# Optimization experiments

Measured on AMD Instinct MI355X. Metric: run time of the kernel, lower is better.

The kernel has to match this reference:

```python
import jax, jax.numpy as jnp
import numpy as np
import math

NHEADS = 4


def _mab(Q, K, qw, qb, kw, kb, vw, vb, ow, ob, mask):
    """MAB2 from tripletformer: multi-head attention (head split via cat(split,0)),
    softmax scale uses sqrt(FULL dim_V), masked_fill(mask==0, -1e10), residual on
    the projected Q, then O + relu(fc_o(O))."""
    dv = qw.shape[1]
    dh = dv // NHEADS
    B, Nq, _ = Q.shape
    Nk = K.shape[1]
    Qh = (Q @ qw + qb).reshape(B, Nq, NHEADS, dh).transpose(0, 2, 1, 3)  # B,h,Nq,dh
    Kh = (K @ kw + kb).reshape(B, Nk, NHEADS, dh).transpose(0, 2, 1, 3)
    Vh = (K @ vw + vb).reshape(B, Nk, NHEADS, dh).transpose(0, 2, 1, 3)
    att = jnp.einsum('bhqd,bhkd->bhqk', Qh, Kh) * (1.0 / math.sqrt(dv))
    att = jnp.where(mask, att, jnp.asarray(-1e10, att.dtype))
    A = jax.nn.softmax(att, axis=-1)
    Oh = Qh + jnp.einsum('bhqk,bhkd->bhqd', A, Vh)
    O = Oh.transpose(0, 2, 1, 3).reshape(B, Nq, dv)
    return O + jax.nn.relu(O @ ow + ob)


def _forward(context_x, value, mask, obs_len, iff_w, iff_b, ind_points,
             q0w, q0b, k0w, k0b, v0w, v0b, o0w, o0b,
             q1w, q1b, k1w, k1b, v1w, v1b, o1w, o1b):
    B, L = context_x.shape
    D = value.shape[-1]
    mflat = mask.reshape(B, L * D)
    # stable stream compaction: observed entries first, original (time-major,
    # channel-minor) order preserved; truncate to static obs_len
    order = jnp.argsort(-mflat, axis=-1, stable=True)[:, :obs_len]  # (B, N)
    T = jnp.broadcast_to(context_x[:, :, None], (B, L, D)).reshape(B, L * D)
    C = jnp.broadcast_to(jnp.arange(D, dtype=jnp.int32), (B, L, D)).reshape(B, L * D)
    U = value.reshape(B, L * D)
    take = lambda a: jnp.take_along_axis(a, order, axis=-1)
    T_, U_, mk_ = take(T), take(U), take(mflat)
    Ch = jax.nn.one_hot(take(C), D, dtype=value.dtype)  # one_hot(num_classes=dim-2)
    X = jnp.concatenate([Ch, T_[..., None], U_[..., None]], axis=-1) * mk_[..., None]
    Y = jax.nn.relu(X @ iff_w + iff_b) * mk_[..., None]
    key_valid = mk_ > 0                        # (B, N)
    mask1 = key_valid[:, None, None, :]        # mab0: mask padded keys
    mask2 = key_valid[:, None, :, None]        # mab1: mask padded query rows
    Z = Y
    n_layers = ind_points.shape[0]
    for i in range(n_layers):
        I = jnp.broadcast_to(ind_points[i], (B,) + ind_points[i].shape)
        H = _mab(I, Z, q0w[i], q0b[i], k0w[i], k0b[i], v0w[i], v0b[i], o0w[i], o0b[i], mask1)
        Zn = _mab(Z, H, q1w[i], q1b[i], k1w[i], k1b[i], v1w[i], v1b[i], o1w[i], o1b[i], mask2)
        Z = Zn * mk_[..., None] + Z
    return Z, mk_[..., None]


def setup_inputs() -> dict:
    B, L, D, OBS, DK, M, NL = 16, 512, 41, 4096, 128, 128, 3
    key = jax.random.key(0)
    ks = jax.random.split(key, 16)
    context_x = jnp.sort(jax.random.uniform(ks[0], (B, L), dtype=jnp.float32), axis=-1)
    value = jax.random.normal(ks[1], (B, L, D), dtype=jnp.float32)
    # exactly OBS observed entries per batch row -> static packed length
    r = jax.random.uniform(ks[2], (B, L * D))
    kth = jnp.sort(r, axis=-1)[:, OBS]
    mask = (r < kth[:, None]).astype(jnp.float32).reshape(B, L, D)

    def w(k, shape, fan):
        return jax.random.normal(k, shape, dtype=jnp.float32) / math.sqrt(fan)

    inp = dict(
        context_x=context_x, value=value, mask=mask, obs_len=OBS,
        iff_w=w(ks[3], (D + 2, DK), D + 2), iff_b=jnp.zeros((DK,), jnp.float32),
        ind_points=w(ks[4], (NL, M, DK), DK),
    )
    for j, n in enumerate(['q0', 'k0', 'v0', 'o0', 'q1', 'k1', 'v1', 'o1']):
        inp[n + 'w'] = w(ks[5 + j], (NL, DK, DK), DK)
        inp[n + 'b'] = jnp.zeros((NL, DK), jnp.float32)
    return inp


def reference(context_x, value, mask, obs_len, iff_w, iff_b, ind_points,
              q0w, q0b, k0w, k0b, v0w, v0b, o0w, o0b,
              q1w, q1b, k1w, k1b, v1w, v1b, o1w, o1b):
    return _forward(context_x, value, mask, obs_len, iff_w, iff_b, ind_points,
                    q0w, q0b, k0w, k0b, v0w, v0b, o0w, o0b,
                    q1w, q1b, k1w, k1b, v1w, v1b, o1w, o1b)
```

## Files before the change

### kernel.cpp

```cpp
#include <hip/hip_runtime.h>
#include <math.h>

#define NBATCH 16
#define SEQL   512
#define DIM    41
#define LDFLAT (SEQL*DIM)
#define OBS    4096
#define DK     128
#define NH     4
#define DH     32

typedef short bf16x8 __attribute__((ext_vector_type(8)));
typedef short short8v __attribute__((ext_vector_type(8)));
typedef float floatx4 __attribute__((ext_vector_type(4)));

__device__ __forceinline__ short f2bf(float f) {
  union { float f; unsigned u; } v;
  v.f = f;
  unsigned r = (v.u + 0x7fffu + ((v.u >> 16) & 1u)) >> 16;
  return (short)r;
}
__device__ __forceinline__ float bf2f(short s) {
  union { unsigned u; float f; } v;
  v.u = ((unsigned)(unsigned short)s) << 16;
  return v.f;
}


__device__ __forceinline__ int swz(int row, int col) {
  return row * 128 + ((((col >> 3) ^ row) & 15) << 3) + (col & 7);
}

typedef struct { int4 v[4]; } WStageH;
__device__ __forceinline__ void stage_load_h(WStageH& s,
                                             const short* __restrict__ Wh,
                                             int tid) {
#pragma unroll
  for (int k = 0; k < 4; k++)
    s.v[k] = *(const int4*)&Wh[(size_t)tid * 8 + (size_t)k * 2048];
}
__device__ __forceinline__ void stage_write_h(short* Wl, const WStageH& s,
                                              int tid) {
#pragma unroll
  for (int k = 0; k < 4; k++) {
    int i = tid * 8 + k * 2048;
    *(int4*)&Wl[swz(i >> 7, i & 127)] = s.v[k];
  }
}
typedef struct { int4 v[2]; } WStageF;
__device__ __forceinline__ void stage_load_f(WStageF& s,
                                             const short* __restrict__ W,
                                             int tid) {
#pragma unroll
  for (int k = 0; k < 2; k++)
    s.v[k] = *(const int4*)&W[(size_t)tid * 8 + (size_t)k * 8192];
}
__device__ __forceinline__ void stage_write_f(short* Wl, const WStageF& s,
                                              int tid) {
#pragma unroll
  for (int k = 0; k < 2; k++) {
    int i = tid * 8 + k * 8192;
    *(int4*)&Wl[swz(i >> 7, i & 127)] = s.v[k];
  }
}

__device__ __forceinline__ void gemm4_s(const short* Wl, const bf16x8 af[4],
                                        int lm, int quad, floatx4 acc[4]) {
#pragma unroll
  for (int nt = 0; nt < 4; nt++) acc[nt] = (floatx4){0.f, 0.f, 0.f, 0.f};
#pragma unroll
  for (int kc = 0; kc < 4; kc++) {
    bf16x8 a = af[kc];
#pragma unroll
    for (int nt = 0; nt < 4; nt++) {
      bf16x8 b = *(const bf16x8*)&Wl[swz(nt * 16 + lm, kc * 32 + quad * 8)];
      acc[nt] = __builtin_amdgcn_mfma_f32_16x16x32_bf16(a, b, acc[nt], 0, 0, 0);
    }
  }
}
__device__ __forceinline__ void gemm2_s(const short* Wl, const bf16x8 af[4],
                                        int colq, int lm, int quad,
                                        floatx4 acc[2]) {
#pragma unroll
  for (int nt = 0; nt < 2; nt++) acc[nt] = (floatx4){0.f, 0.f, 0.f, 0.f};
#pragma unroll
  for (int kc = 0; kc < 4; kc++) {
    bf16x8 a = af[kc];
#pragma unroll
    for (int nt = 0; nt < 2; nt++) {
      bf16x8 b = *(const bf16x8*)&Wl[swz(colq * 32 + nt * 16 + lm,
                                         kc * 32 + quad * 8)];
      acc[nt] = __builtin_amdgcn_mfma_f32_16x16x32_bf16(a, b, acc[nt], 0, 0, 0);
    }
  }
}
__device__ __forceinline__ void load_af_s(const short* Xl, int strip, int lm,
                                          int quad, bf16x8 af[4]) {
#pragma unroll
  for (int kc = 0; kc < 4; kc++)
    af[kc] = *(const bf16x8*)&Xl[swz(strip * 16 + lm, kc * 32 + quad * 8)];
}
__device__ __forceinline__ void store_sl4(short* Sl, const floatx4 acc[4],
                                          const float* __restrict__ bias,
                                          int wv, int lm, int quad,
                                          int colbase) {
#pragma unroll
  for (int nt = 0; nt < 4; nt++) {
    int col = colbase + nt * 16 + lm;
    float bn = bias[col];
#pragma unroll
    for (int r = 0; r < 4; r++)
      Sl[swz(wv * 16 + quad * 4 + r, col)] = f2bf(acc[nt][r] + bn);
  }
}
__device__ __forceinline__ void write_hs_s(const short* Sl,
                                           short* __restrict__ out, int rb,
                                           int nshift, int tid) {
  int rr = tid >> 2, hh = tid & 3;
  int r = rb + rr;
  int bb = r >> nshift, nn = r & ((1 << nshift) - 1);
  size_t o = (((size_t)(bb * NH + hh) << nshift) + nn) * 32;
#pragma unroll
  for (int j = 0; j < 4; j++)
    *(int4*)&out[o + j * 8] = *(int4*)&Sl[swz(rr, hh * 32 + j * 8)];
}
__device__ __forceinline__ void write_hs_q(const short* Sl,
                                           short* __restrict__ out, int rb,
                                           int nshift, int strip, int colq,
                                           int lane) {
  int rr = strip * 16 + (lane >> 2);
  int r = rb + rr;
  int bb = r >> nshift, nn = r & ((1 << nshift) - 1);
  size_t o = (((size_t)(bb * NH + colq) << nshift) + nn) * 32 + (lane & 3) * 8;
  *(int4*)&out[o] = *(const int4*)&Sl[swz(rr, colq * 32 + (lane & 3) * 8)];
}

__global__ __launch_bounds__(1024) void prep_build_kernel(
    const float* __restrict__ q0w, const float* __restrict__ k0w,
    const float* __restrict__ v0w, const float* __restrict__ o0w,
    const float* __restrict__ q1w, const float* __restrict__ k1w,
    const float* __restrict__ v1w, const float* __restrict__ o1w,
    short* __restrict__ Wt,
    const float* __restrict__ mask, int* __restrict__ order,
    float* __restrict__ mk_out, float* __restrict__ mk_out2) {
  __shared__ float Tl[128 * 132];
  __shared__ int c_ones[21];
  __shared__ int base_ones[21];
  __shared__ int base_zeros[21];
  __shared__ int s_total;
  int tid = threadIdx.x;

  if (blockIdx.x < 24) {
    int id = blockIdx.x, l = id >> 3, wi = id & 7;
    const float* s;
    switch (wi) {
      case 0: s = q0w; break; case 1: s = k0w; break;
      case 2: s = v0w; break; case 3: s = o0w; break;
      case 4: s = q1w; break; case 5: s = k1w; break;
      case 6: s = v1w; break; default: s = o1w; break;
    }
    s += (size_t)l * 16384;
    for (int i = tid * 4; i < 16384; i += 4096) {
      int k = i >> 7, n = i & 127;
      float4 x = *(const float4*)&s[i];
      Tl[k * 132 + n + 0] = x.x; Tl[k * 132 + n + 1] = x.y;
      Tl[k * 132 + n + 2] = x.z; Tl[k * 132 + n + 3] = x.w;
    }
    __syncthreads();
    short* dst = Wt + (size_t)id * 16384;
    int n = tid >> 3, k0 = (tid & 7) * 16;
    for (int jc = 0; jc < 2; jc++) {
      short8v t;
#pragma unroll
      for (int j = 0; j < 8; j++) t[j] = f2bf(Tl[(k0 + jc * 8 + j) * 132 + n]);
      *(short8v*)&dst[n * 128 + k0 + jc * 8] = t;
    }
    return;
  }

  int b = blockIdx.x - 24;
  const float* m = mask + (size_t)b * LDFLAT;
  int lane = tid & 63, w = tid >> 6;

  for (int ch = w; ch < 21; ch += 16) {
    int cnt = 0;
    for (int off = lane; off < 1024; off += 64) {
      int j = ch * 1024 + off;
      if (j < LDFLAT) cnt += (m[j] > 0.f) ? 1 : 0;
    }
    for (int o = 32; o > 0; o >>= 1) cnt += __shfl_xor(cnt, o);
    if (lane == 0) c_ones[ch] = cnt;
  }
  __syncthreads();
  if (tid == 0) {
    int ro = 0, rz = 0, tot = 0;
    for (int ch = 0; ch < 21; ch++) tot += c_ones[ch];
    for (int ch = 0; ch < 21; ch++) {
      base_ones[ch] = ro; base_zeros[ch] = rz;
      int cv = (ch == 20) ? (LDFLAT - 20 * 1024) : 1024;
      ro += c_ones[ch]; rz += cv - c_ones[ch];
    }
    s_total = tot;
  }
  __syncthreads();
  int total_ones = s_total;
  for (int ch = w; ch < 21; ch += 16) {
    int obase = base_ones[ch], zbase = base_zeros[ch];
    int climit = (ch == 20) ? (LDFLAT - 20 * 1024) : 1024;
    int run_ones = 0;
    for (int off0 = 0; off0 < climit; off0 += 64) {
      int off = off0 + lane;
      bool valid = off < climit;
      int j = ch * 1024 + off;
      float mv = valid ? m[j] : 0.f;
      int one = (valid && mv > 0.f) ? 1 : 0;
      int v = one;
      for (int o = 1; o < 64; o <<= 1) {
        int t = __shfl_up(v, (unsigned)o);
        if (lane >= o) v += t;
      }
      int wave_ones = __shfl(v, 63);
      if (valid) {
        int ones_before = run_ones + (v - one);
        int pos = one ? (obase + ones_before)
                      : (total_ones + zbase + (off - ones_before));
        if (pos < OBS) {
          order[b * OBS + pos] = j;
          mk_out[b * OBS + pos] = mv;
          mk_out2[b * OBS + pos] = mv;
        }
      }
      run_ones += wave_ones;
    }
  }
}

__global__ __launch_bounds__(256, 3) void fusedA_kernel(
    const int* __restrict__ order, const float* __restrict__ mk_g,
    const float* __restrict__ cx, const float* __restrict__ value,
    const float* __restrict__ iff_w, const float* __restrict__ iff_b,
    float* __restrict__ Z,
    const short* __restrict__ Wk, const float* __restrict__ kbias,
    short* __restrict__ Kb,
    const short* __restrict__ Wv, const float* __restrict__ vbias,
    short* __restrict__ Vb,
    const short* __restrict__ Wq, const float* __restrict__ qbias,
    short* __restrict__ Qb,
    const float* __restrict__ indp, const short* __restrict__ WtAll,
    const float* __restrict__ q0b_all, short* __restrict__ qh_b) {
  __shared__ __align__(16) short Xl[64 * 128];
  __shared__ __align__(16) short WlA[64 * 128];
  __shared__ __align__(16) short WlB[64 * 128];
  int tid = threadIdx.x;
  int wv = tid >> 6, lane = tid & 63, lm = lane & 15, quad = lane >> 4;
  int r_l = lane >> 2, seg = lane & 3;
  int lrow = wv * 16 + r_l;

  if (blockIdx.x >= 1024) {
    int id = blockIdx.x - 1024;
    int l = id >> 1, rbq = (id & 1) * 64;
    const float* X = indp + (size_t)l * 16384 + (size_t)rbq * 128;
    const short* W = WtAll + (size_t)(l * 8) * 16384;
    const float* bias = q0b_all + (size_t)l * 128;
    short* out = qh_b + (size_t)l * 16384;
    WStageH sA, sB;
    stage_load_h(sA, W, tid);
    stage_load_h(sB, W + 8192, tid);
    const float* Xr = X + (size_t)lrow * 128;
#pragma unroll
    for (int jj = 0; jj < 8; jj++) {
      int col = seg * 32 + jj * 4;
      float4 x = *(const float4*)&Xr[col];
      *(short4*)&Xl[swz(lrow, col)] =
          make_short4(f2bf(x.x), f2bf(x.y), f2bf(x.z), f2bf(x.w));
    }
    stage_write_h(WlA, sA, tid);
    stage_write_h(WlB, sB, tid);
    __syncthreads();
    bf16x8 af[4];
    load_af_s(Xl, wv, lm, quad, af);
    floatx4 acc[4];
    gemm4_s(WlA, af, lm, quad, acc);
    store_sl4(Xl, acc, bias, wv, lm, quad, 0);
    gemm4_s(WlB, af, lm, quad, acc);
    store_sl4(Xl, acc, bias, wv, lm, quad, 64);
    write_hs_s(Xl, out, rbq, 7, tid);
    return;
  }

  int rb = blockIdx.x * 64;
  WStageH s0; stage_load_h(s0, Wk, tid);
  int grow = rb + lrow;
  int bb = grow >> 12;
  int j = order[grow];
  int l = j / DIM, d = j - l * DIM;
  float t = cx[bb * SEQL + l];
  float u = value[(size_t)bb * LDFLAT + j];
  float mkv = mk_g[grow];
#pragma unroll
  for (int jj = 0; jj < 8; jj++) {
    int col = seg * 32 + jj * 4;
    float4 w0 = *(const float4*)&iff_w[d * DK + col];
    float4 w1 = *(const float4*)&iff_w[41 * DK + col];
    float4 w2 = *(const float4*)&iff_w[42 * DK + col];
    float4 b4 = *(const float4*)&iff_b[col];
    float4 z;
    z.x = fmaxf(w0.x + t * w1.x + u * w2.x + b4.x, 0.f) * mkv;
    z.y = fmaxf(w0.y + t * w1.y + u * w2.y + b4.y, 0.f) * mkv;
    z.z = fmaxf(w0.z + t * w1.z + u * w2.z + b4.z, 0.f) * mkv;
    z.w = fmaxf(w0.w + t * w1.w + u * w2.w + b4.w, 0.f) * mkv;
    *(float4*)&Z[(size_t)grow * DK + col] = z;
    *(short4*)&Xl[swz(lrow, col)] =
        make_short4(f2bf(z.x), f2bf(z.y), f2bf(z.z), f2bf(z.w));
  }
  stage_write_h(WlA, s0, tid);
  __syncthreads();
  WStageH s1; stage_load_h(s1, Wk + 8192, tid);
  bf16x8 af[4];
  load_af_s(Xl, wv, lm, quad, af);
  floatx4 acc[4];
  gemm4_s(WlA, af, lm, quad, acc);
  store_sl4(Xl, acc, kbias, wv, lm, quad, 0);
  stage_write_h(WlB, s1, tid);
  __syncthreads();
  WStageH s2; stage_load_h(s2, Wv, tid);
  gemm4_s(WlB, af, lm, quad, acc);
  store_sl4(Xl, acc, kbias, wv, lm, quad, 64);
  write_hs_s(Xl, Kb, rb, 12, tid);
  stage_write_h(WlA, s2, tid);
  __syncthreads();
  WStageH s3; stage_load_h(s3, Wv + 8192, tid);
  gemm4_s(WlA, af, lm, quad, acc);
  store_sl4(Xl, acc, vbias, wv, lm, quad, 0);
  stage_write_h(WlB, s3, tid);
  __syncthreads();
  WStageH s4; stage_load_h(s4, Wq, tid);
  gemm4_s(WlB, af, lm, quad, acc);
  store_sl4(Xl, acc, vbias, wv, lm, quad, 64);
  write_hs_s(Xl, Vb, rb, 12, tid);
  stage_write_h(WlA, s4, tid);
  __syncthreads();
  WStageH s5; stage_load_h(s5, Wq + 8192, tid);
  gemm4_s(WlA, af, lm, quad, acc);
  store_sl4(Xl, acc, qbias, wv, lm, quad, 0);
  stage_write_h(WlB, s5, tid);
  __syncthreads();
  gemm4_s(WlB, af, lm, quad, acc);
  store_sl4(Xl, acc, qbias, wv, lm, quad, 64);
  write_hs_s(Xl, Qb, rb, 12, tid);
}

__global__ __launch_bounds__(256) void attn1_kernel(
    const short* __restrict__ Qh,
    const short* __restrict__ Kh, const short* __restrict__ Vh,
    const float* __restrict__ mk,
    float* __restrict__ Opart, float* __restrict__ mpart,
    float* __restrict__ lpart) {
  __shared__ __align__(16) short Ql[128 * 40];
  __shared__ __align__(16) short Kc[64 * 40];
  __shared__ __align__(16) short Vtc[32 * 74];
  __shared__ __align__(16) short Pl[128 * 72];
  __shared__ float mkc[64];
  int bh = blockIdx.x;
  int b = bh >> 2, h = bh & 3;
  int ks = blockIdx.y;
  int tid = threadIdx.x;
  int wv = tid >> 6, lane = tid & 63, lm = lane & 15, quad = lane >> 4;

  const float scale = 0.08838834764831845f;
  const short* kbase = Kh + ((size_t)bh * OBS + ks * 512) * 32;
  const short* vbase = Vh + ((size_t)bh * OBS + ks * 512) * 32;
  const float* mkb = mk + (size_t)b * OBS + ks * 512;

  int i0 = tid * 8;
  int r0 = i0 >> 5, cv = i0 & 31;
  int4 kreg = *(const int4*)&kbase[i0];
  int4 vreg = *(const int4*)&vbase[i0];
  float mreg = (tid < 64) ? mkb[tid] : 0.f;

  const short* qbg = Qh + (size_t)h * 128 * 32;
  for (int i = tid * 8; i < 128 * 32; i += 2048) {
    int r = i >> 5, c = i & 31;
    *(int4*)&Ql[r * 40 + c] = *(const int4*)&qbg[i];
  }
  __syncthreads();
  bf16x8 aq[2];
  aq[0] = *(bf16x8*)&Ql[(wv * 32 + lm) * 40 + quad * 8];
  aq[1] = *(bf16x8*)&Ql[(wv * 32 + 16 + lm) * 40 + quad * 8];

  float m_i[2][4], l_i[2][4];
  floatx4 oacc[2][2];
#pragma unroll
  for (int mt = 0; mt < 2; mt++) {
#pragma unroll
    for (int r = 0; r < 4; r++) { m_i[mt][r] = -1e30f; l_i[mt][r] = 0.f; }
    oacc[mt][0] = (floatx4){0.f, 0.f, 0.f, 0.f};
    oacc[mt][1] = (floatx4){0.f, 0.f, 0.f, 0.f};
  }

  for (int ch = 0; ch < 8; ch++) {
    __syncthreads();
    *(int4*)&Kc[r0 * 40 + cv] = kreg;
    {
      short* vv = (short*)&vreg;
#pragma unroll
      for (int j = 0; j < 8; j++) Vtc[(cv + j) * 74 + r0] = vv[j];
    }
    if (tid < 64) mkc[tid] = mreg;
    if (ch < 7) {
      kreg = *(const int4*)&kbase[(ch + 1) * 2048 + i0];
      vreg = *(const int4*)&vbase[(ch + 1) * 2048 + i0];
      if (tid < 64) mreg = mkb[(ch + 1) * 64 + tid];
    }
    __syncthreads();

    floatx4 sf[2][4];
#pragma unroll
    for (int nt = 0; nt < 4; nt++) {
      bf16x8 bfrag = *(bf16x8*)&Kc[(nt * 16 + lm) * 40 + quad * 8];
      floatx4 z = {0.f, 0.f, 0.f, 0.f};
      sf[0][nt] = __builtin_amdgcn_mfma_f32_16x16x32_bf16(aq[0], bfrag, z, 0, 0, 0);
      sf[1][nt] = __builtin_amdgcn_mfma_f32_16x16x32_bf16(aq[1], bfrag, z, 0, 0, 0);
    }
#pragma unroll
    for (int nt = 0; nt < 4; nt++) {
      float mkv = mkc[nt * 16 + lm];
      bool ok = mkv > 0.f;
#pragma unroll
      for (int mt = 0; mt < 2; mt++)
#pragma unroll
        for (int r = 0; r < 4; r++)
          sf[mt][nt][r] = ok ? sf[mt][nt][r] * scale : -1e10f;
    }
#pragma unroll
    for (int mt = 0; mt < 2; mt++) {
#pragma unroll
      for (int r = 0; r < 4; r++) {
        float mx = fmaxf(fmaxf(sf[mt][0][r], sf[mt][1][r]),
                         fmaxf(sf[mt][2][r], sf[mt][3][r]));
        mx = fmaxf(mx, __shfl_xor(mx, 1));
        mx = fmaxf(mx, __shfl_xor(mx, 2));
        mx = fmaxf(mx, __shfl_xor(mx, 4));
        mx = fmaxf(mx, __shfl_xor(mx, 8));
        float mn = fmaxf(m_i[mt][r], mx);
        float al = __expf(m_i[mt][r] - mn);
        float ps = 0.f;
#pragma unroll
        for (int nt = 0; nt < 4; nt++) {
          float p = __expf(sf[mt][nt][r] - mn);
          sf[mt][nt][r] = p;
          ps += p;
        }
        ps += __shfl_xor(ps, 1);
        ps += __shfl_xor(ps, 2);
        ps += __shfl_xor(ps, 4);
        ps += __shfl_xor(ps, 8);
        l_i[mt][r] = l_i[mt][r] * al + ps;
        m_i[mt][r] = mn;
        oacc[mt][0] *= al;
        oacc[mt][1] *= al;
      }
    }
#pragma unroll
    for (int mt = 0; mt < 2; mt++)
#pragma unroll
      for (int nt = 0; nt < 4; nt++)
#pragma unroll
        for (int r = 0; r < 4; r++)
          Pl[(wv * 32 + mt * 16 + quad * 4 + r) * 72 + nt * 16 + lm] =
              f2bf(sf[mt][nt][r]);
#pragma unroll
    for (int kc = 0; kc < 2; kc++) {
      bf16x8 vf0 = *(bf16x8*)&Vtc[lm * 74 + kc * 32 + quad * 8];
      bf16x8 vf1 = *(bf16x8*)&Vtc[(16 + lm) * 74 + kc * 32 + quad * 8];
#pragma unroll
      for (int mt = 0; mt < 2; mt++) {
        bf16x8 pf = *(bf16x8*)&Pl[(wv * 32 + mt * 16 + lm) * 72 + kc * 32 + quad * 8];
        oacc[mt][0] = __builtin_amdgcn_mfma_f32_16x16x32_bf16(pf, vf0, oacc[mt][0], 0, 0, 0);
        oacc[mt][1] = __builtin_amdgcn_mfma_f32_16x16x32_bf16(pf, vf1, oacc[mt][1], 0, 0, 0);
      }
    }
  }
  float* ob = Opart + (size_t)(ks * 64 + bh) * 128 * 32;
#pragma unroll
  for (int mt = 0; mt < 2; mt++) {
#pragma unroll
    for (int r = 0; r < 4; r++) {
      int row = wv * 32 + mt * 16 + quad * 4 + r;
      ob[(size_t)row * 32 + lm] = oacc[mt][0][r];
      ob[(size_t)row * 32 + 16 + lm] = oacc[mt][1][r];
      if (lm == 0) {
        mpart[(size_t)(ks * 64 + bh) * 128 + row] = m_i[mt][r];
        lpart[(size_t)(ks * 64 + bh) * 128 + row] = l_i[mt][r];
      }
    }
  }
}

__global__ __launch_bounds__(1024) void fusedB_kernel(
    const float* __restrict__ Opart, const float* __restrict__ mpart,
    const float* __restrict__ lpart, const short* __restrict__ qh,
    const short* __restrict__ Wo, const float* __restrict__ obias,
    const short* __restrict__ Wk, const float* __restrict__ kbias,
    const short* __restrict__ Wv, const float* __restrict__ vbias,
    short* __restrict__ khb, short* __restrict__ vhb) {
  __shared__ __align__(16) short Xl[64 * 128];
  __shared__ __align__(16) short WlA[128 * 128];
  __shared__ __align__(16) short WlB[128 * 128];
  int tid = threadIdx.x;
  int rb = blockIdx.x * 64;
  int b = rb >> 7, n0 = rb & 127;
  int wv = tid >> 6, lane = tid & 63, lm = lane & 15, quad = lane >> 4;
  int strip = wv & 3, colq = wv >> 2;
  WStageF sWo; stage_load_f(sWo, Wo, tid);
#pragma unroll
  for (int p = 0; p < 2; p++) {
    int slot = p * 1024 + tid;
    int pair = slot >> 3;
    int hh = pair & 3, rr = pair >> 2;
    int c4 = (slot & 7) * 4;
    int n = n0 + rr;
    int bh = b * 4 + hh;
    float mv[8], lv[8], m = -1e30f;
#pragma unroll
    for (int s = 0; s < 8; s++) {
      mv[s] = mpart[(size_t)(s * 64 + bh) * 128 + n];
      lv[s] = lpart[(size_t)(s * 64 + bh) * 128 + n];
      m = fmaxf(m, mv[s]);
    }
    float l = 0.f, oa0 = 0.f, oa1 = 0.f, oa2 = 0.f, oa3 = 0.f;
#pragma unroll
    for (int s = 0; s < 8; s++) {
      float w = __expf(mv[s] - m);
      l += lv[s] * w;
      float4 v = *(const float4*)&Opart[((size_t)(s * 64 + bh) * 128 + n) * 32 + c4];
      oa0 += v.x * w; oa1 += v.y * w; oa2 += v.z * w; oa3 += v.w * w;
    }
    float li = 1.f / l;
    int2 qi = *(const int2*)&qh[((size_t)hh * 128 + n) * 32 + c4];
    const short* qs = (const short*)&qi;
    short4 o4;
    o4.x = f2bf(bf2f(qs[0]) + oa0 * li);
    o4.y = f2bf(bf2f(qs[1]) + oa1 * li);
    o4.z = f2bf(bf2f(qs[2]) + oa2 * li);
    o4.w = f2bf(bf2f(qs[3]) + oa3 * li);
    *(short4*)&Xl[swz(rr, hh * 32 + c4)] = o4;
  }
  stage_write_f(WlA, sWo, tid);
  __syncthreads();
  bf16x8 afO[4];
  load_af_s(Xl, strip, lm, quad, afO);
  __syncthreads();
  WStageF sWk; stage_load_f(sWk, Wk, tid);
  floatx4 acc[2];
  gemm2_s(WlA, afO, colq, lm, quad, acc);
#pragma unroll
  for (int nt = 0; nt < 2; nt++) {
    int col = colq * 32 + nt * 16 + lm;
    float bn = obias[col];
#pragma unroll
    for (int r = 0; r < 4; r++) {
      int row = strip * 16 + quad * 4 + r;
      float ov = bf2f(Xl[swz(row, col)]);
      Xl[swz(row, col)] = f2bf(ov + fmaxf(acc[nt][r] + bn, 0.f));
    }
  }
  stage_write_f(WlB, sWk, tid);
  __syncthreads();
  bf16x8 afH[4];
  load_af_s(Xl, strip, lm, quad, afH);
  __syncthreads();
  WStageF sWv; stage_load_f(sWv, Wv, tid);
  gemm2_s(WlB, afH, colq, lm, quad, acc);
#pragma unroll
  for (int nt = 0; nt < 2; nt++) {
    int col = colq * 32 + nt * 16 + lm;
    float bn = kbias[col];
#pragma unroll
    for (int r = 0; r < 4; r++)
      Xl[swz(strip * 16 + quad * 4 + r, col)] = f2bf(acc[nt][r] + bn);
  }
  write_hs_q(Xl, khb, rb, 7, strip, colq, lane);
  stage_write_f(WlA, sWv, tid);
  __syncthreads();
  gemm2_s(WlA, afH, colq, lm, quad, acc);
#pragma unroll
  for (int nt = 0; nt < 2; nt++) {
    int col = colq * 32 + nt * 16 + lm;
    float bn = vbias[col];
#pragma unroll
    for (int r = 0; r < 4; r++)
      Xl[swz(strip * 16 + quad * 4 + r, col)] = f2bf(acc[nt][r] + bn);
  }
  write_hs_q(Xl, vhb, rb, 7, strip, colq, lane);
}

__global__ __launch_bounds__(256, 4) void attn2_kernel(
    const short* __restrict__ Qh, const short* __restrict__ Kh,
    const short* __restrict__ Vh, short* __restrict__ O) {
  __shared__ __align__(16) short Kl[128 * 40];
  __shared__ __align__(16) short Vt[32 * 136];
  __shared__ __align__(16) short Ql[64 * 40];
  __shared__ __align__(16) short Pl[64 * 128];
  int bh = blockIdx.x;
  int b = bh >> 2, h = bh & 3;
  int q0 = blockIdx.y * 64;
  int tid = threadIdx.x;
  int wv = tid >> 6, lane = tid & 63, lm = lane & 15, quad = lane >> 4;
  const short* kb = Kh + (size_t)bh * 128 * 32;
  const short* vb = Vh + (size_t)bh * 128 * 32;
  const short* qb = Qh + ((size_t)bh * OBS + q0) * 32;

  for (int i = tid * 8; i < 128 * 32; i += 2048) {
    int r = i >> 5, c = i & 31;
    *(int4*)&Kl[r * 40 + c] = *(const int4*)&kb[i];
  }
  for (int i = tid * 8; i < 64 * 32; i += 2048) {
    int r = i >> 5, c = i & 31;
    *(int4*)&Ql[r * 40 + c] = *(const int4*)&qb[i];
  }
  for (int i = tid * 8; i < 128 * 32; i += 2048) {
    int r = i >> 5, c = i & 31;
    int4 vv4 = *(const int4*)&vb[i];
    short* vv = (short*)&vv4;
#pragma unroll
    for (int j = 0; j < 8; j++) Vt[(c + j) * 136 + r] = vv[j];
  }
  __syncthreads();

  const float scale = 0.08838834764831845f;
  bf16x8 afrag = *(bf16x8*)&Ql[(wv * 16 + lm) * 40 + quad * 8];
  floatx4 sf[8];
#pragma unroll
  for (int nt = 0; nt < 8; nt++) {
    bf16x8 bfrag = *(bf16x8*)&Kl[(nt * 16 + lm) * 40 + quad * 8];
    floatx4 z = {0.f, 0.f, 0.f, 0.f};
    sf[nt] = __builtin_amdgcn_mfma_f32_16x16x32_bf16(afrag, bfrag, z, 0, 0, 0);
  }
#pragma unroll
  for (int nt = 0; nt < 8; nt++) sf[nt] *= scale;
  float linv[4];
#pragma unroll
  for (int r = 0; r < 4; r++) {
    float mx = sf[0][r];
#pragma unroll
    for (int nt = 1; nt < 8; nt++) mx = fmaxf(mx, sf[nt][r]);
    mx = fmaxf(mx, __shfl_xor(mx, 1));
    mx = fmaxf(mx, __shfl_xor(mx, 2));
    mx = fmaxf(mx, __shfl_xor(mx, 4));
    mx = fmaxf(mx, __shfl_xor(mx, 8));
    float sum = 0.f;
#pragma unroll
    for (int nt = 0; nt < 8; nt++) {
      float p = __expf(sf[nt][r] - mx);
      sf[nt][r] = p;
      sum += p;
    }
    sum += __shfl_xor(sum, 1);
    sum += __shfl_xor(sum, 2);
    sum += __shfl_xor(sum, 4);
    sum += __shfl_xor(sum, 8);
    linv[r] = 1.f / sum;
  }
#pragma unroll
  for (int nt = 0; nt < 8; nt++)
#pragma unroll
    for (int r = 0; r < 4; r++)
      Pl[swz(wv * 16 + quad * 4 + r, nt * 16 + lm)] = f2bf(sf[nt][r]);

  floatx4 oacc[2] = {{0.f, 0.f, 0.f, 0.f}, {0.f, 0.f, 0.f, 0.f}};
#pragma unroll
  for (int kc = 0; kc < 4; kc++) {
    bf16x8 pf = *(bf16x8*)&Pl[swz(wv * 16 + lm, kc * 32 + quad * 8)];
#pragma unroll
    for (int nt2 = 0; nt2 < 2; nt2++) {
      bf16x8 vf = *(bf16x8*)&Vt[(nt2 * 16 + lm) * 136 + kc * 32 + quad * 8];
      oacc[nt2] = __builtin_amdgcn_mfma_f32_16x16x32_bf16(pf, vf, oacc[nt2], 0, 0, 0);
    }
  }
  short* Ol = Pl;
#pragma unroll
  for (int nt2 = 0; nt2 < 2; nt2++) {
#pragma unroll
    for (int r = 0; r < 4; r++) {
      int qrow = wv * 16 + quad * 4 + r;
      float q = bf2f(Ql[qrow * 40 + nt2 * 16 + lm]);
      Ol[swz(qrow, nt2 * 16 + lm)] = f2bf(q + oacc[nt2][r] * linv[r]);
    }
  }
  int rr = tid >> 2, seg = tid & 3;
  size_t o = ((size_t)b * OBS + q0 + rr) * 128 + h * 32 + seg * 8;
  *(int4*)&O[o] = *(int4*)&Ol[swz(rr, seg * 8)];
}

__global__ __launch_bounds__(256, 3) void fusedC_kernel(
    const short* __restrict__ Ob, const short* __restrict__ Wo,
    const float* __restrict__ obias, const float* __restrict__ mk,
    const float* __restrict__ Zin, float* __restrict__ Zout,
    const short* __restrict__ Wk, const float* __restrict__ kbias,
    short* __restrict__ Kb,
    const short* __restrict__ Wv, const float* __restrict__ vbias,
    short* __restrict__ Vb,
    const short* __restrict__ Wq, const float* __restrict__ qbias,
    short* __restrict__ Qb) {
  __shared__ __align__(16) short Xl[64 * 128];
  __shared__ __align__(16) short WlA[64 * 128];
  __shared__ __align__(16) short WlB[64 * 128];
  int tid = threadIdx.x;
  int rb = blockIdx.x * 64;
  int wv = tid >> 6, lane = tid & 63, lm = lane & 15, quad = lane >> 4;

  WStageH s0; stage_load_h(s0, Wo, tid);
  bf16x8 afO[4];
  {
    const short* arow = Ob + (size_t)(rb + wv * 16 + lm) * 128;
#pragma unroll
    for (int kc = 0; kc < 4; kc++) {
      afO[kc] = *(const bf16x8*)&arow[kc * 32 + quad * 8];
      *(bf16x8*)&Xl[swz(wv * 16 + lm, kc * 32 + quad * 8)] = afO[kc];
    }
  }
  int row0 = wv * 16 + quad * 4;
  float mkv[4];
#pragma unroll
  for (int r = 0; r < 4; r++) mkv[r] = mk[rb + row0 + r];
  stage_write_h(WlA, s0, tid);
  __syncthreads();
  WStageH s1; stage_load_h(s1, Wo + 8192, tid);
  floatx4 acc[4];
  gemm4_s(WlA, afO, lm, quad, acc);
#pragma unroll
  for (int nt = 0; nt < 4; nt++) {
    int col = nt * 16 + lm;
    float bn = obias[col];
#pragma unroll
    for (int r = 0; r < 4; r++) {
      int row = row0 + r;
      size_t g = (size_t)(rb + row) * 128 + col;
      float ov = bf2f(Xl[swz(row, col)]);
      float f = ov + fmaxf(acc[nt][r] + bn, 0.f);
      float zv = Zin[g] + f * mkv[r];
      Zout[g] = zv;
      Xl[swz(row, col)] = f2bf(zv);
    }
  }
  stage_write_h(WlB, s1, tid);
  __syncthreads();
  WStageH s2;
  if (Wk) stage_load_h(s2, Wk, tid);
  gemm4_s(WlB, afO, lm, quad, acc);
#pragma unroll
  for (int nt = 0; nt < 4; nt++) {
    int col = 64 + nt * 16 + lm;
    float bn = obias[col];
#pragma unroll
    for (int r = 0; r < 4; r++) {
      int row = row0 + r;
      size_t g = (size_t)(rb + row) * 128 + col;
      float ov = bf2f(Xl[swz(row, col)]);
      float f = ov + fmaxf(acc[nt][r] + bn, 0.f);
      float zv = Zin[g] + f * mkv[r];
      Zout[g] = zv;
      Xl[swz(row, col)] = f2bf(zv);
    }
  }
  if (Wk == nullptr) return;
  bf16x8 af[4];
  load_af_s(Xl, wv, lm, quad, af);
  stage_write_h(WlA, s2, tid);
  __syncthreads();
  WStageH s3; stage_load_h(s3, Wk + 8192, tid);
  gemm4_s(WlA, af, lm, quad, acc);
  store_sl4(Xl, acc, kbias, wv, lm, quad, 0);
  stage_write_h(WlB, s3, tid);
  __syncthreads();
  WStageH s4; stage_load_h(s4, Wv, tid);
  gemm4_s(WlB, af, lm, quad, acc);
  store_sl4(Xl, acc, kbias, wv, lm, quad, 64);
  write_hs_s(Xl, Kb, rb, 12, tid);
  stage_write_h(WlA, s4, tid);
  __syncthreads();
  WStageH s5; stage_load_h(s5, Wv + 8192, tid);
  gemm4_s(WlA, af, lm, quad, acc);
  store_sl4(Xl, acc, vbias, wv, lm, quad, 0);
  stage_write_h(WlB, s5, tid);
  __syncthreads();
  WStageH s6; stage_load_h(s6, Wq, tid);
  gemm4_s(WlB, af, lm, quad, acc);
  store_sl4(Xl, acc, vbias, wv, lm, quad, 64);
  write_hs_s(Xl, Vb, rb, 12, tid);
  stage_write_h(WlA, s6, tid);
  __syncthreads();
  WStageH s7; stage_load_h(s7, Wq + 8192, tid);
  gemm4_s(WlA, af, lm, quad, acc);
  store_sl4(Xl, acc, qbias, wv, lm, quad, 0);
  stage_write_h(WlB, s7, tid);
  __syncthreads();
  gemm4_s(WlB, af, lm, quad, acc);
  store_sl4(Xl, acc, qbias, wv, lm, quad, 64);
  write_hs_s(Xl, Qb, rb, 12, tid);
}

extern "C" void kernel_launch(void* const* d_in, const int* in_sizes, int n_in,
                              void* d_out, int out_size, void* d_ws,
                              size_t ws_size, hipStream_t stream) {
  const float* cx    = (const float*)d_in[0];
  const float* value = (const float*)d_in[1];
  const float* mask  = (const float*)d_in[2];
  const float* iff_w = (const float*)d_in[4];
  const float* iff_b = (const float*)d_in[5];
  const float* indp  = (const float*)d_in[6];
  const float* q0w = (const float*)d_in[7];  const float* q0b = (const float*)d_in[8];
  const float* k0w = (const float*)d_in[9];  const float* k0b = (const float*)d_in[10];
  const float* v0w = (const float*)d_in[11]; const float* v0b = (const float*)d_in[12];
  const float* o0w = (const float*)d_in[13]; const float* o0b = (const float*)d_in[14];
  const float* q1w = (const float*)d_in[15]; const float* q1b = (const float*)d_in[16];
  const float* k1w = (const float*)d_in[17]; const float* k1b = (const float*)d_in[18];
  const float* v1w = (const float*)d_in[19]; const float* v1b = (const float*)d_in[20];
  const float* o1w = (const float*)d_in[21]; const float* o1b = (const float*)d_in[22];

  char* ws = (char*)d_ws;
  short* Wt    = (short*)ws;  ws += (size_t)24 * 16384 * 2;
  int*   order = (int*)ws;    ws += (size_t)NBATCH * OBS * 4;
  float* mk_g  = (float*)ws;  ws += (size_t)NBATCH * OBS * 4;
  float* Z     = (float*)ws;  ws += (size_t)NBATCH * OBS * DK * 4;
  short* Qb    = (short*)ws;  ws += (size_t)NBATCH * OBS * DK * 2;
  short* Kb    = (short*)ws;  ws += (size_t)NBATCH * OBS * DK * 2;
  short* Vb    = (short*)ws;  ws += (size_t)NBATCH * OBS * DK * 2;
  short* Ob    = (short*)ws;  ws += (size_t)NBATCH * OBS * DK * 2;
  short* qh_b  = (short*)ws;  ws += (size_t)3 * 128 * DK * 2;
  short* khb   = (short*)ws;  ws += (size_t)NBATCH * NH * 128 * DH * 2;
  short* vhb   = (short*)ws;  ws += (size_t)NBATCH * NH * 128 * DH * 2;
  float* Opart = (float*)ws;  ws += (size_t)8 * 64 * 128 * 32 * 4;
  float* mpart = (float*)ws;  ws += (size_t)8 * 64 * 128 * 4;
  float* lpart = (float*)ws;  ws += (size_t)8 * 64 * 128 * 4;

  float* outZ  = (float*)d_out;
  float* outMk = outZ + (size_t)NBATCH * OBS * DK;

  prep_build_kernel<<<40, 1024, 0, stream>>>(q0w, k0w, v0w, o0w, q1w, k1w,
                                             v1w, o1w, Wt, mask, order, mk_g,
                                             outMk);

  const short* W[3][8];
  for (int l = 0; l < 3; l++)
    for (int wi = 0; wi < 8; wi++) W[l][wi] = Wt + (size_t)(l * 8 + wi) * 16384;

  fusedA_kernel<<<1030, 256, 0, stream>>>(
      order, mk_g, cx, value, iff_w, iff_b, Z,
      W[0][1], k0b, Kb, W[0][2], v0b, Vb, W[0][4], q1b, Qb,
      indp, Wt, q0b, qh_b);

  for (int l = 0; l < 3; l++) {
    attn1_kernel<<<dim3(64, 8), 256, 0, stream>>>(
        qh_b + (size_t)l * 16384, Kb, Vb, mk_g, Opart, mpart, lpart);
    fusedB_kernel<<<32, 1024, 0, stream>>>(
        Opart, mpart, lpart, qh_b + (size_t)l * 16384,
        W[l][3], o0b + (size_t)l * 128,
        W[l][5], k1b + (size_t)l * 128,
        W[l][6], v1b + (size_t)l * 128, khb, vhb);
    attn2_kernel<<<dim3(64, 64), 256, 0, stream>>>(Qb, khb, vhb, Ob);
    if (l < 2) {
      fusedC_kernel<<<1024, 256, 0, stream>>>(
          Ob, W[l][7], o1b + (size_t)l * 128, mk_g, Z, Z,
          W[l + 1][1], k0b + (size_t)(l + 1) * 128, Kb,
          W[l + 1][2], v0b + (size_t)(l + 1) * 128, Vb,
          W[l + 1][4], q1b + (size_t)(l + 1) * 128, Qb);
    } else {
      fusedC_kernel<<<1024, 256, 0, stream>>>(
          Ob, W[l][7], o1b + (size_t)l * 128, mk_g, Z, outZ,
          nullptr, nullptr, nullptr, nullptr, nullptr, nullptr,
          nullptr, nullptr, nullptr);
    }
  }
}
```

Before: 459.8 us.

## Fuse second attention into the output-projection kernel, dropping the O buffer

Merges attn2 into fusedC. Each 64-row block loops over the four heads, computing per-head attention into shared memory with double-buffered register prefetch of the next head's K/V/Q. It then runs the output projection and the next layer's K/V/Q projections. This removes a kernel launch and the bf16 O round trip through global memory. In exchange, each block recomputes the K/V staging per head, shares one LDS union across phases, and writes the new Q in place over the input Q buffer. Those in-place writes look safe only because each block reads only its own rows.

```diff
diff --git a/kernel.cpp b/kernel.cpp
--- a/kernel.cpp
+++ b/kernel.cpp
@@ -595,137 +595,147 @@
   write_hs_q(Xl, vhb, rb, 7, strip, colq, lane);
 }
 
-__global__ __launch_bounds__(256, 4) void attn2_kernel(
-    const short* __restrict__ Qh, const short* __restrict__ Kh,
-    const short* __restrict__ Vh, short* __restrict__ O) {
-  __shared__ __align__(16) short Kl[128 * 40];
-  __shared__ __align__(16) short Vt[32 * 136];
-  __shared__ __align__(16) short Ql[64 * 40];
-  __shared__ __align__(16) short Pl[64 * 128];
-  int bh = blockIdx.x;
-  int b = bh >> 2, h = bh & 3;
-  int q0 = blockIdx.y * 64;
-  int tid = threadIdx.x;
-  int wv = tid >> 6, lane = tid & 63, lm = lane & 15, quad = lane >> 4;
-  const short* kb = Kh + (size_t)bh * 128 * 32;
-  const short* vb = Vh + (size_t)bh * 128 * 32;
-  const short* qb = Qh + ((size_t)bh * OBS + q0) * 32;
-
-  for (int i = tid * 8; i < 128 * 32; i += 2048) {
-    int r = i >> 5, c = i & 31;
-    *(int4*)&Kl[r * 40 + c] = *(const int4*)&kb[i];
-  }
-  for (int i = tid * 8; i < 64 * 32; i += 2048) {
-    int r = i >> 5, c = i & 31;
-    *(int4*)&Ql[r * 40 + c] = *(const int4*)&qb[i];
-  }
-  for (int i = tid * 8; i < 128 * 32; i += 2048) {
-    int r = i >> 5, c = i & 31;
-    int4 vv4 = *(const int4*)&vb[i];
-    short* vv = (short*)&vv4;
-#pragma unroll
-    for (int j = 0; j < 8; j++) Vt[(c + j) * 136 + r] = vv[j];
-  }
-  __syncthreads();
-
-  const float scale = 0.08838834764831845f;
-  bf16x8 afrag = *(bf16x8*)&Ql[(wv * 16 + lm) * 40 + quad * 8];
-  floatx4 sf[8];
-#pragma unroll
-  for (int nt = 0; nt < 8; nt++) {
-    bf16x8 bfrag = *(bf16x8*)&Kl[(nt * 16 + lm) * 40 + quad * 8];
-    floatx4 z = {0.f, 0.f, 0.f, 0.f};
-    sf[nt] = __builtin_amdgcn_mfma_f32_16x16x32_bf16(afrag, bfrag, z, 0, 0, 0);
-  }
-#pragma unroll
-  for (int nt = 0; nt < 8; nt++) sf[nt] *= scale;
-  float linv[4];
-#pragma unroll
-  for (int r = 0; r < 4; r++) {
-    float mx = sf[0][r];
-#pragma unroll
-    for (int nt = 1; nt < 8; nt++) mx = fmaxf(mx, sf[nt][r]);
-    mx = fmaxf(mx, __shfl_xor(mx, 1));
-    mx = fmaxf(mx, __shfl_xor(mx, 2));
-    mx = fmaxf(mx, __shfl_xor(mx, 4));
-    mx = fmaxf(mx, __shfl_xor(mx, 8));
-    float sum = 0.f;
-#pragma unroll
-    for (int nt = 0; nt < 8; nt++) {
-      float p = __expf(sf[nt][r] - mx);
-      sf[nt][r] = p;
-      sum += p;
-    }
-    sum += __shfl_xor(sum, 1);
-    sum += __shfl_xor(sum, 2);
-    sum += __shfl_xor(sum, 4);
-    sum += __shfl_xor(sum, 8);
-    linv[r] = 1.f / sum;
-  }
-#pragma unroll
-  for (int nt = 0; nt < 8; nt++)
-#pragma unroll
-    for (int r = 0; r < 4; r++)
-      Pl[swz(wv * 16 + quad * 4 + r, nt * 16 + lm)] = f2bf(sf[nt][r]);
-
-  floatx4 oacc[2] = {{0.f, 0.f, 0.f, 0.f}, {0.f, 0.f, 0.f, 0.f}};
-#pragma unroll
-  for (int kc = 0; kc < 4; kc++) {
-    bf16x8 pf = *(bf16x8*)&Pl[swz(wv * 16 + lm, kc * 32 + quad * 8)];
-#pragma unroll
-    for (int nt2 = 0; nt2 < 2; nt2++) {
-      bf16x8 vf = *(bf16x8*)&Vt[(nt2 * 16 + lm) * 136 + kc * 32 + quad * 8];
-      oacc[nt2] = __builtin_amdgcn_mfma_f32_16x16x32_bf16(pf, vf, oacc[nt2], 0, 0, 0);
-    }
-  }
-  short* Ol = Pl;
-#pragma unroll
-  for (int nt2 = 0; nt2 < 2; nt2++) {
-#pragma unroll
-    for (int r = 0; r < 4; r++) {
-      int qrow = wv * 16 + quad * 4 + r;
-      float q = bf2f(Ql[qrow * 40 + nt2 * 16 + lm]);
-      Ol[swz(qrow, nt2 * 16 + lm)] = f2bf(q + oacc[nt2][r] * linv[r]);
-    }
-  }
-  int rr = tid >> 2, seg = tid & 3;
-  size_t o = ((size_t)b * OBS + q0 + rr) * 128 + h * 32 + seg * 8;
-  *(int4*)&O[o] = *(int4*)&Ol[swz(rr, seg * 8)];
-}
-
-__global__ __launch_bounds__(256, 3) void fusedC_kernel(
-    const short* __restrict__ Ob, const short* __restrict__ Wo,
-    const float* __restrict__ obias, const float* __restrict__ mk,
+__global__ __launch_bounds__(256, 3) void attn2c_kernel(
+    short* Qh,
+    const short* __restrict__ Kh, const short* __restrict__ Vh,
+    const short* __restrict__ Wo, const float* __restrict__ obias,
+    const float* __restrict__ mk,
     const float* __restrict__ Zin, float* __restrict__ Zout,
     const short* __restrict__ Wk, const float* __restrict__ kbias,
     short* __restrict__ Kb,
     const short* __restrict__ Wv, const float* __restrict__ vbias,
     short* __restrict__ Vb,
-    const short* __restrict__ Wq, const float* __restrict__ qbias,
-    short* __restrict__ Qb) {
+    const short* __restrict__ Wq, const float* __restrict__ qbias) {
+  __shared__ __align__(16) short U[17664];
   __shared__ __align__(16) short Xl[64 * 128];
-  __shared__ __align__(16) short WlA[64 * 128];
-  __shared__ __align__(16) short WlB[64 * 128];
+  short* Kc  = U;
+  short* Vtc = U + 5120;
+  short* Pl  = U + 9472;
+  short* WlA = U;
+  short* WlB = U + 8192;
   int tid = threadIdx.x;
   int rb = blockIdx.x * 64;
+  int b = rb >> 12, q0 = rb & 4095;
   int wv = tid >> 6, lane = tid & 63, lm = lane & 15, quad = lane >> 4;
-
-  WStageH s0; stage_load_h(s0, Wo, tid);
-  bf16x8 afO[4];
-  {
-    const short* arow = Ob + (size_t)(rb + wv * 16 + lm) * 128;
-#pragma unroll
-    for (int kc = 0; kc < 4; kc++) {
-      afO[kc] = *(const bf16x8*)&arow[kc * 32 + quad * 8];
-      *(bf16x8*)&Xl[swz(wv * 16 + lm, kc * 32 + quad * 8)] = afO[kc];
-    }
-  }
+  const float scale = 0.08838834764831845f;
+  int i0 = tid * 8;
+  int r0 = i0 >> 5, c0 = i0 & 31;
+
   int row0 = wv * 16 + quad * 4;
   float mkv[4];
 #pragma unroll
   for (int r = 0; r < 4; r++) mkv[r] = mk[rb + row0 + r];
+
+  const short* kb0 = Kh + (((size_t)(b * NH)) << 7) * 32;
+  const short* vb0 = Vh + (((size_t)(b * NH)) << 7) * 32;
+  const short* qb0 = Qh + ((((size_t)(b * NH)) << 12) + q0) * 32;
+  int4 kreg0 = *(const int4*)&kb0[i0];
+  int4 kreg1 = *(const int4*)&kb0[2048 + i0];
+  int4 vreg0 = *(const int4*)&vb0[i0];
+  int4 vreg1 = *(const int4*)&vb0[2048 + i0];
+  bf16x8 aq = *(const bf16x8*)&qb0[(wv * 16 + lm) * 32 + quad * 8];
+  int4 qres = *(const int4*)&qb0[(wv * 16 + (lane >> 2)) * 32 + (lane & 3) * 8];
+
+  WStageH s0;
+  for (int h = 0; h < NH; h++) {
+    __syncthreads();
+    *(int4*)&Kc[r0 * 40 + c0] = kreg0;
+    *(int4*)&Kc[(r0 + 64) * 40 + c0] = kreg1;
+    {
+      short* vv = (short*)&vreg0;
+#pragma unroll
+      for (int j = 0; j < 8; j++) Vtc[(c0 + j) * 136 + r0] = vv[j];
+      vv = (short*)&vreg1;
+#pragma unroll
+      for (int j = 0; j < 8; j++) Vtc[(c0 + j) * 136 + r0 + 64] = vv[j];
+    }
+    bf16x8 aqn; int4 qresn;
+    if (h < 3) {
+      const short* kbn = Kh + (((size_t)(b * NH + h + 1)) << 7) * 32;
+      const short* vbn = Vh + (((size_t)(b * NH + h + 1)) << 7) * 32;
+      kreg0 = *(const int4*)&kbn[i0];
+      kreg1 = *(const int4*)&kbn[2048 + i0];
+      vreg0 = *(const int4*)&vbn[i0];
+      vreg1 = *(const int4*)&vbn[2048 + i0];
+      const short* qbn = Qh + ((((size_t)(b * NH + h + 1)) << 12) + q0) * 32;
+      aqn = *(const bf16x8*)&qbn[(wv * 16 + lm) * 32 + quad * 8];
+      qresn = *(const int4*)&qbn[(wv * 16 + (lane >> 2)) * 32 + (lane & 3) * 8];
+    } else {
+      stage_load_h(s0, Wo, tid);
+    }
+    __syncthreads();
+
+    floatx4 sf[8];
+#pragma unroll
+    for (int nt = 0; nt < 8; nt++) {
+      bf16x8 bfrag = *(const bf16x8*)&Kc[(nt * 16 + lm) * 40 + quad * 8];
+      floatx4 z = {0.f, 0.f, 0.f, 0.f};
+      sf[nt] = __builtin_amdgcn_mfma_f32_16x16x32_bf16(aq, bfrag, z, 0, 0, 0);
+    }
+#pragma unroll
+    for (int nt = 0; nt < 8; nt++) sf[nt] *= scale;
+    float linv[4];
+#pragma unroll
+    for (int r = 0; r < 4; r++) {
+      float mx = sf[0][r];
+#pragma unroll
+      for (int nt = 1; nt < 8; nt++) mx = fmaxf(mx, sf[nt][r]);
+      mx = fmaxf(mx, __shfl_xor(mx, 1));
+      mx = fmaxf(mx, __shfl_xor(mx, 2));
+      mx = fmaxf(mx, __shfl_xor(mx, 4));
+      mx = fmaxf(mx, __shfl_xor(mx, 8));
+      float sum = 0.f;
+#pragma unroll
+      for (int nt = 0; nt < 8; nt++) {
+        float p = __expf(sf[nt][r] - mx);
+        sf[nt][r] = p;
+        sum += p;
+      }
+      sum += __shfl_xor(sum, 1);
+      sum += __shfl_xor(sum, 2);
+      sum += __shfl_xor(sum, 4);
+      sum += __shfl_xor(sum, 8);
+      linv[r] = 1.f / sum;
+    }
+#pragma unroll
+    for (int nt = 0; nt < 8; nt++)
+#pragma unroll
+      for (int r = 0; r < 4; r++)
+        Pl[swz(wv * 16 + quad * 4 + r, nt * 16 + lm)] = f2bf(sf[nt][r]);
+
+    floatx4 oacc[2] = {{0.f, 0.f, 0.f, 0.f}, {0.f, 0.f, 0.f, 0.f}};
+#pragma unroll
+    for (int kc = 0; kc < 4; kc++) {
+      bf16x8 pf = *(const bf16x8*)&Pl[swz(wv * 16 + lm, kc * 32 + quad * 8)];
+#pragma unroll
+      for (int nt2 = 0; nt2 < 2; nt2++) {
+        bf16x8 vf = *(const bf16x8*)&Vtc[(nt2 * 16 + lm) * 136 + kc * 32 + quad * 8];
+        oacc[nt2] = __builtin_amdgcn_mfma_f32_16x16x32_bf16(pf, vf, oacc[nt2], 0, 0, 0);
+      }
+    }
+    float* Pw = (float*)(Pl + wv * 2048);
+#pragma unroll
+    for (int nt2 = 0; nt2 < 2; nt2++)
+#pragma unroll
+      for (int r = 0; r < 4; r++)
+        Pw[(quad * 4 + r) * 32 + nt2 * 16 + lm] = oacc[nt2][r] * linv[r];
+    {
+      int rl = lane >> 2, c8 = (lane & 3) * 8;
+      const float* Pf = (const float*)(Pl + wv * 2048);
+      const short* qs = (const short*)&qres;
+      int4 o4; short* os = (short*)&o4;
+#pragma unroll
+      for (int j = 0; j < 8; j++)
+        os[j] = f2bf(Pf[rl * 32 + c8 + j] + bf2f(qs[j]));
+      *(int4*)&Xl[swz(wv * 16 + rl, h * 32 + c8)] = o4;
+    }
+    if (h < 3) { aq = aqn; qres = qresn; }
+  }
+  __syncthreads();
   stage_write_h(WlA, s0, tid);
   __syncthreads();
+  bf16x8 afO[4];
+  load_af_s(Xl, wv, lm, quad, afO);
   WStageH s1; stage_load_h(s1, Wo + 8192, tid);
   floatx4 acc[4];
   gemm4_s(WlA, afO, lm, quad, acc);
@@ -798,7 +808,7 @@
   __syncthreads();
   gemm4_s(WlB, af, lm, quad, acc);
   store_sl4(Xl, acc, qbias, wv, lm, quad, 64);
-  write_hs_s(Xl, Qb, rb, 12, tid);
+  write_hs_s(Xl, Qh, rb, 12, tid);
 }
 
 extern "C" void kernel_launch(void* const* d_in, const int* in_sizes, int n_in,
@@ -827,7 +837,6 @@
   short* Qb    = (short*)ws;  ws += (size_t)NBATCH * OBS * DK * 2;
   short* Kb    = (short*)ws;  ws += (size_t)NBATCH * OBS * DK * 2;
   short* Vb    = (short*)ws;  ws += (size_t)NBATCH * OBS * DK * 2;
-  short* Ob    = (short*)ws;  ws += (size_t)NBATCH * OBS * DK * 2;
   short* qh_b  = (short*)ws;  ws += (size_t)3 * 128 * DK * 2;
   short* khb   = (short*)ws;  ws += (size_t)NBATCH * NH * 128 * DH * 2;
   short* vhb   = (short*)ws;  ws += (size_t)NBATCH * NH * 128 * DH * 2;
@@ -859,18 +868,17 @@
         W[l][3], o0b + (size_t)l * 128,
         W[l][5], k1b + (size_t)l * 128,
         W[l][6], v1b + (size_t)l * 128, khb, vhb);
-    attn2_kernel<<<dim3(64, 64), 256, 0, stream>>>(Qb, khb, vhb, Ob);
     if (l < 2) {
-      fusedC_kernel<<<1024, 256, 0, stream>>>(
-          Ob, W[l][7], o1b + (size_t)l * 128, mk_g, Z, Z,
+      attn2c_kernel<<<1024, 256, 0, stream>>>(
+          Qb, khb, vhb, W[l][7], o1b + (size_t)l * 128, mk_g, Z, Z,
           W[l + 1][1], k0b + (size_t)(l + 1) * 128, Kb,
           W[l + 1][2], v0b + (size_t)(l + 1) * 128, Vb,
-          W[l + 1][4], q1b + (size_t)(l + 1) * 128, Qb);
+          W[l + 1][4], q1b + (size_t)(l + 1) * 128);
     } else {
-      fusedC_kernel<<<1024, 256, 0, stream>>>(
-          Ob, W[l][7], o1b + (size_t)l * 128, mk_g, Z, outZ,
+      attn2c_kernel<<<1024, 256, 0, stream>>>(
+          Qb, khb, vhb, W[l][7], o1b + (size_t)l * 128, mk_g, Z, outZ,
           nullptr, nullptr, nullptr, nullptr, nullptr, nullptr,
-          nullptr, nullptr, nullptr);
-    }
-  }
-}
+          nullptr, nullptr);
+    }
+  }
+}
```

Result: slower. 496.5 us (+8.0%).
